# Performance work log

Hardware: AMD Instinct MI355X
Metric: run time of the kernel (lower is better)

## Reference

```python
import jax, jax.numpy as jnp
import numpy as np

B, S, H = 32, 2048, 1024

def setup_inputs() -> dict:
    key = jax.random.key(0)
    k1, k2, k3, k4, k5 = jax.random.split(key, 5)
    return {
        "hidden": jax.random.normal(k1, (B, H), dtype=jnp.float32),
        "encoder_outputs": jax.random.normal(k2, (B, S, H), dtype=jnp.float32),
        "W_attn": jax.random.normal(k3, (H, H), dtype=jnp.float32) * (1.0 / np.sqrt(H)),
        "b_attn": jax.random.normal(k4, (H,), dtype=jnp.float32) * 0.01,
        "v": jax.random.uniform(k5, (H,), dtype=jnp.float32),
    }

def reference(hidden, encoder_outputs, W_attn, b_attn, v):
    # energy = tanh((enc + hidden[:,None,:]) @ W^T + b)  -> [B,S,H]
    x = encoder_outputs + hidden[:, None, :]
    energy = jnp.tanh(jnp.einsum('bsh,oh->bso', x, W_attn) + b_attn)
    scores = jnp.einsum('bsh,h->bs', energy, v)            # [B,S]
    attn_weights = jax.nn.softmax(scores, axis=1)          # [B,S]
    context = jnp.einsum('bs,bsh->bh', attn_weights, encoder_outputs)  # [B,H]
    return (context, attn_weights)
```

## Files before the change

### kernel.cpp

```cpp
#include <hip/hip_runtime.h>
#include <hip/hip_bf16.h>

#define BATCH 32
#define SEQ   2048
#define HID   1024
#define M_TOT (BATCH*SEQ)
#define NG    32

typedef __attribute__((ext_vector_type(8))) short          bf16x8;
typedef __attribute__((ext_vector_type(8))) unsigned short us8;
typedef __attribute__((ext_vector_type(4))) float          f32x4;

__device__ __forceinline__ unsigned short f2bf_rn(float x) {
    unsigned u = __float_as_uint(x);
    return (unsigned short)((u + 0x7fffu + ((u >> 16) & 1u)) >> 16);
}
__device__ __forceinline__ float bf2f(unsigned short h) {
    return __uint_as_float(((unsigned)h) << 16);
}

using as1_cv = const __attribute__((address_space(1))) void;
using as3_v  = __attribute__((address_space(3))) void;
__device__ __forceinline__ void gload16(const void* g, char* s) {
    __builtin_amdgcn_global_load_lds((as1_cv*)g, (as3_v*)s, 16, 0, 0);
}

#define FENCE() asm volatile("" ::: "memory")
#define BAR_LG() do { asm volatile("s_waitcnt lgkmcnt(0)" ::: "memory"); \
                      __builtin_amdgcn_s_barrier(); FENCE(); } while (0)
#define BAR_VM4() do { asm volatile("s_waitcnt vmcnt(4) lgkmcnt(0)" ::: "memory"); \
                       __builtin_amdgcn_s_barrier(); FENCE(); } while (0)

#define MFMA_BLK(A4, B4, IB) do { \
  _Pragma("unroll") for (int i_ = 0; i_ < 4; i_++) \
  _Pragma("unroll") for (int j_ = 0; j_ < 4; j_++) \
    acc[(IB) + i_][j_] = __builtin_amdgcn_mfma_f32_16x16x32_bf16(A4[i_], B4[j_], acc[(IB)+i_][j_], 0, 0, 0); \
} while (0)

__global__ __launch_bounds__(256) void k_convW(const float* __restrict__ W,
                                               unsigned short* __restrict__ w2) {
    const int i8 = (blockIdx.x * 256 + threadIdx.x) * 8;
    const int o = i8 >> 10, h = i8 & 1023;
    float4 w0 = *(const float4*)(W + i8);
    float4 w1 = *(const float4*)(W + i8 + 4);
    float xs[8] = {w0.x, w0.y, w0.z, w0.w, w1.x, w1.y, w1.z, w1.w};
    us8 hv{}, lv{};
#pragma unroll
    for (int t = 0; t < 8; t++) {
        unsigned short xh = f2bf_rn(xs[t]);
        hv[t] = (unsigned short)xh;
        lv[t] = (unsigned short)f2bf_rn(xs[t] - bf2f(xh));
    }
    *(us8*)(w2 + (size_t)o * 2048 + h)        = hv;
    *(us8*)(w2 + (size_t)o * 2048 + 1024 + h) = lv;
}

__global__ __launch_bounds__(512, 2) void k_gemm_scores(
    const float* __restrict__ enc,
    const float* __restrict__ hidden,
    const unsigned short* __restrict__ w2,
    const float* __restrict__ b_attn,
    const float* __restrict__ v,
    float* __restrict__ pscore16)
{
    extern __shared__ char smem[];
    float* hidL = (float*)(smem + 131072);

    const int tid  = threadIdx.x;
    const int lane = tid & 63, wid = tid >> 6;
    const int wr = wid >> 2, wc = wid & 3;
    const int fr = lane & 15, g = lane >> 4;
    const int gxr = (fr >> 1) & 3;
    const int gsw = (g ^ gxr) * 16;

    const int bid  = blockIdx.x;
    const int swz  = (bid & 7) * 128 + (bid >> 3);
    const int mbase = (swz >> 2) * 256;
    const int nbase = (swz & 3) * 256;
    const int bidx  = mbase >> 11;

    const int arow = tid >> 1;
    const int acol = (tid & 1) * 16;
    const int axr  = (arow >> 1) & 3;
    const int ao0  = (((tid & 1) * 2) ^ axr) * 16;
    const int ao1  = ao0 ^ 16;
    const float* encP = enc + (size_t)(mbase + arow) * HID + acol;

    const int brow  = wid * 16 + (lane >> 2);
    const int bsx8  = ((lane & 3) ^ ((lane >> 3) & 3)) * 8;

    *(float2*)(hidL + tid * 2) = *(const float2*)(hidden + (size_t)bidx * HID + tid * 2);

    f32x4 acc[8][4];
#pragma unroll
    for (int i = 0; i < 8; i++)
#pragma unroll
        for (int j = 0; j < 4; j++) acc[i][j] = (f32x4)0.f;

    float4 er[4];

    auto loadEnc = [&](int Gn) {
        const float* ep = encP + Gn * 32;
#pragma unroll
        for (int q = 0; q < 4; q++) er[q] = *(const float4*)(ep + q * 4);
    };
    auto convA = [&](int Gn) {
        char* ap = smem + (Gn & 1) * 32768 + arow * 64;
        const float* hp = hidL + Gn * 32 + acol;
        us8 hv0{}, hv1{}, lv0{}, lv1{};
#pragma unroll
        for (int q = 0; q < 4; q++) {
            float4 e = er[q];
            float4 h = *(const float4*)(hp + q * 4);
            float xs[4] = {e.x + h.x, e.y + h.y, e.z + h.z, e.w + h.w};
#pragma unroll
            for (int t = 0; t < 4; t++) {
                unsigned short xh = f2bf_rn(xs[t]);
                unsigned short xl = f2bf_rn(xs[t] - bf2f(xh));
                const int p = q * 4 + t;
                if (p < 8) { hv0[p] = xh; lv0[p] = xl; }
                else       { hv1[p - 8] = xh; lv1[p - 8] = xl; }
            }
        }
        *(us8*)(ap + ao0)          = hv0;
        *(us8*)(ap + ao1)          = hv1;
        *(us8*)(ap + 16384 + ao0)  = lv0;
        *(us8*)(ap + 16384 + ao1)  = lv1;
    };
    auto stageB = [&](int G2, int part) {
        const unsigned short* s0 = w2 + (size_t)(nbase + brow) * 2048 + part * 1024 + G2 * 32 + bsx8;
        char* d0 = smem + 65536 + (G2 & 1) * 32768 + part * 16384 + wid * 1024;
        gload16(s0, d0);
        gload16(s0 + (size_t)128 * 2048, d0 + 8192);
    };
    auto rdA = [&](int slot, int part, int i) -> bf16x8 {
        return *(const bf16x8*)(smem + slot * 32768 + part * 16384 +
                                (wr * 128 + i * 16 + fr) * 64 + gsw);
    };
    auto rdB = [&](int slot, int part, int j) -> bf16x8 {
        return *(const bf16x8*)(smem + 65536 + slot * 32768 + part * 16384 +
                                (wc * 64 + j * 16 + fr) * 64 + gsw);
    };

    loadEnc(0);
    stageB(0, 0); stageB(0, 1);
    stageB(1, 0); stageB(1, 1);
    asm volatile("s_waitcnt lgkmcnt(0)" ::: "memory");
    __builtin_amdgcn_s_barrier(); FENCE();
    convA(0);
    loadEnc(1);

    bf16x8 aa[4], bh[4], bl[4];

    for (int G = 0; G < NG; ++G) {
        const int slot = G & 1;
        BAR_VM4();
#pragma unroll
        for (int i = 0; i < 4; i++) aa[i] = rdA(slot, 0, i);
#pragma unroll
        for (int j = 0; j < 4; j++) bh[j] = rdB(slot, 0, j);
#pragma unroll
        for (int j = 0; j < 4; j++) bl[j] = rdB(slot, 1, j);
        __builtin_amdgcn_s_setprio(1);
        MFMA_BLK(aa, bh, 0);
        __builtin_amdgcn_s_setprio(0);
        BAR_LG();
        if (G + 2 < NG) stageB(G + 2, 0);
        __builtin_amdgcn_s_setprio(1);
        MFMA_BLK(aa, bl, 0);
        __builtin_amdgcn_s_setprio(0);
        BAR_LG();
#pragma unroll
        for (int i = 0; i < 4; i++) aa[i] = rdA(slot, 0, 4 + i);
        if (G + 2 < NG) stageB(G + 2, 1);
        __builtin_amdgcn_s_setprio(1);
        MFMA_BLK(aa, bh, 4);
        __builtin_amdgcn_s_setprio(0);
        BAR_LG();
        if (G + 1 < NG) convA(G + 1);
        if (G + 2 < NG) loadEnc(G + 2);
        __builtin_amdgcn_s_setprio(1);
        MFMA_BLK(aa, bl, 4);
        __builtin_amdgcn_s_setprio(0);
        BAR_LG();
#pragma unroll
        for (int i = 0; i < 4; i++) aa[i] = rdA(slot, 1, i);
        __builtin_amdgcn_s_setprio(1);
        MFMA_BLK(aa, bh, 0);
        __builtin_amdgcn_s_setprio(0);
        BAR_LG();
#pragma unroll
        for (int i = 0; i < 4; i++) aa[i] = rdA(slot, 1, 4 + i);
        __builtin_amdgcn_s_setprio(1);
        MFMA_BLK(aa, bh, 4);
        __builtin_amdgcn_s_setprio(0);
    }

    float rs[8][4];
#pragma unroll
    for (int i = 0; i < 8; i++)
#pragma unroll
        for (int r = 0; r < 4; r++) rs[i][r] = 0.f;

#pragma unroll
    for (int j = 0; j < 4; j++) {
        const int n = nbase + wc * 64 + j * 16 + fr;
        const float ba = b_attn[n];
        const float vv = v[n];
#pragma unroll
        for (int i = 0; i < 8; i++)
#pragma unroll
            for (int r = 0; r < 4; r++) {
                float e  = acc[i][j][r] + ba;
                float ex = __expf(2.f * e);
                rs[i][r] += (1.f - 2.f / (ex + 1.f)) * vv;
            }
    }
#pragma unroll
    for (int off = 1; off < 16; off <<= 1)
#pragma unroll
        for (int i = 0; i < 8; i++)
#pragma unroll
            for (int r = 0; r < 4; r++) rs[i][r] += __shfl_xor(rs[i][r], off, 64);

    float v0 = 0.f, v1 = 0.f;
#pragma unroll
    for (int i = 0; i < 4; i++)
#pragma unroll
        for (int r = 0; r < 4; r++)
            if (fr == i * 4 + r) { v0 = rs[i][r]; v1 = rs[i + 4][r]; }

    const int plane = (swz & 3) * 4 + wc;
    const size_t pb = (size_t)plane * M_TOT + mbase + wr * 128 + g * 4 + (fr & 3);
    pscore16[pb + (fr >> 2) * 16]      = v0;
    pscore16[pb + (fr >> 2) * 16 + 64] = v1;
}

__global__ __launch_bounds__(256) void k_softmax(const float* __restrict__ ps,
                                                 float* __restrict__ out) {
    const int b = blockIdx.x, t = threadIdx.x;
    __shared__ float red[8];
    float loc[8];
    float lmax = -1e30f;
#pragma unroll
    for (int i = 0; i < 8; i++) {
        const int s = t + i * 256;
        float sc = 0.f;
#pragma unroll
        for (int p = 0; p < 16; p++) sc += ps[(size_t)p * M_TOT + (size_t)b * SEQ + s];
        loc[i] = sc;
        lmax = fmaxf(lmax, sc);
    }
    for (int o = 32; o; o >>= 1) lmax = fmaxf(lmax, __shfl_xor(lmax, o, 64));
    if ((t & 63) == 0) red[t >> 6] = lmax;
    __syncthreads();
    const float bmax = fmaxf(fmaxf(red[0], red[1]), fmaxf(red[2], red[3]));
    float ev[8], lsum = 0.f;
#pragma unroll
    for (int i = 0; i < 8; i++) { ev[i] = expf(loc[i] - bmax); lsum += ev[i]; }
    for (int o = 32; o; o >>= 1) lsum += __shfl_xor(lsum, o, 64);
    __syncthreads();
    if ((t & 63) == 0) red[4 + (t >> 6)] = lsum;
    __syncthreads();
    const float inv = 1.f / (red[4] + red[5] + red[6] + red[7]);
#pragma unroll
    for (int i = 0; i < 8; i++)
        out[(size_t)BATCH * HID + (size_t)b * SEQ + t + i * 256] = ev[i] * inv;
}

__global__ __launch_bounds__(256) void k_pctx(const float* __restrict__ enc,
                                              const float* __restrict__ attn,
                                              float* __restrict__ pctx) {
    const int hc = blockIdx.x, scb = blockIdx.y, b = blockIdx.z;
    const int h = hc * 256 + threadIdx.x;
    const float* ap = attn + (size_t)b * SEQ + scb * 256;
    const float* ep = enc + ((size_t)b * SEQ + scb * 256) * HID + h;
    float a = 0.f;
#pragma unroll 4
    for (int s = 0; s < 256; s++) a += ap[s] * ep[(size_t)s * HID];
    pctx[((size_t)scb * BATCH + b) * HID + h] = a;
}

__global__ __launch_bounds__(256) void k_ctx(const float* __restrict__ pctx,
                                             float* __restrict__ out) {
    const int i = blockIdx.x * 256 + threadIdx.x;
    float a = 0.f;
#pragma unroll
    for (int p = 0; p < 8; p++) a += pctx[(size_t)p * BATCH * HID + i];
    out[i] = a;
}

extern "C" void kernel_launch(void* const* d_in, const int* in_sizes, int n_in,
                              void* d_out, int out_size, void* d_ws, size_t ws_size,
                              hipStream_t stream) {
    const float* hidden = (const float*)d_in[0];
    const float* enc    = (const float*)d_in[1];
    const float* W      = (const float*)d_in[2];
    const float* b_attn = (const float*)d_in[3];
    const float* v      = (const float*)d_in[4];
    float* out = (float*)d_out;

    char* ws = (char*)d_ws;
    unsigned short* w2 = (unsigned short*)ws;
    float* pscore16    = (float*)(ws + ((size_t)4 << 20));
    float* pctx        = (float*)ws;

    const int smemBytes = 131072 + 4096;
    hipFuncSetAttribute((const void*)k_gemm_scores,
                        hipFuncAttributeMaxDynamicSharedMemorySize, smemBytes);

    k_convW<<<dim3(512), dim3(256), 0, stream>>>(W, w2);
    k_gemm_scores<<<dim3(1024), dim3(512), smemBytes, stream>>>(
        enc, hidden, w2, b_attn, v, pscore16);
    k_softmax<<<dim3(BATCH), dim3(256), 0, stream>>>(pscore16, out);
    k_pctx<<<dim3(4, 8, BATCH), dim3(256), 0, stream>>>(enc, out + BATCH * HID, pctx);
    k_ctx<<<dim3(128), dim3(256), 0, stream>>>(pctx, out);
}
```

Baseline: 453.5 us.

## Loosen barriers, double-buffer A fragments, and use packed bf16 conversion

The bf16 hi/lo split of the A tile now uses the hardware packed v_cvt_pk_bf16_f32 instruction in place of scalar bit-manipulation rounding. Inside the main loop, several barriers no longer wait on lgkmcnt(0) and one barrier is removed entirely. A second A-fragment register set lets LDS reads overlap with the MFMAs that are still running. Loads and stages are now issued every iteration (clamped indices, so redundant ones occur at the tail) so the vmcnt(8) wait count stays uniform. The changes aim to cut conversion ALU work and barrier stalls, at the cost of more registers, redundant tail loads, and a race risk if the weaker barriers fail to order the LDS writes from convA before the later reads.

```diff
diff --git a/kernel.cpp b/kernel.cpp
--- a/kernel.cpp
+++ b/kernel.cpp
@@ -18,6 +18,11 @@
 __device__ __forceinline__ float bf2f(unsigned short h) {
     return __uint_as_float(((unsigned)h) << 16);
 }
+__device__ __forceinline__ unsigned cvt_pk_bf16(float s0, float s1) {
+    unsigned r;
+    asm("v_cvt_pk_bf16_f32 %0, %1, %2" : "=v"(r) : "v"(s0), "v"(s1));
+    return r;
+}
 
 using as1_cv = const __attribute__((address_space(1))) void;
 using as3_v  = __attribute__((address_space(3))) void;
@@ -26,9 +31,10 @@
 }
 
 #define FENCE() asm volatile("" ::: "memory")
+#define BAR_P()  do { FENCE(); __builtin_amdgcn_s_barrier(); FENCE(); } while (0)
 #define BAR_LG() do { asm volatile("s_waitcnt lgkmcnt(0)" ::: "memory"); \
                       __builtin_amdgcn_s_barrier(); FENCE(); } while (0)
-#define BAR_VM4() do { asm volatile("s_waitcnt vmcnt(4) lgkmcnt(0)" ::: "memory"); \
+#define BAR_VM8() do { asm volatile("s_waitcnt vmcnt(8) lgkmcnt(0)" ::: "memory"); \
                        __builtin_amdgcn_s_barrier(); FENCE(); } while (0)
 
 #define MFMA_BLK(A4, B4, IB) do { \
@@ -107,25 +113,28 @@
     auto convA = [&](int Gn) {
         char* ap = smem + (Gn & 1) * 32768 + arow * 64;
         const float* hp = hidL + Gn * 32 + acol;
-        us8 hv0{}, hv1{}, lv0{}, lv1{};
+        unsigned hpk[8], lpk[8];
 #pragma unroll
         for (int q = 0; q < 4; q++) {
             float4 e = er[q];
             float4 h = *(const float4*)(hp + q * 4);
-            float xs[4] = {e.x + h.x, e.y + h.y, e.z + h.z, e.w + h.w};
-#pragma unroll
-            for (int t = 0; t < 4; t++) {
-                unsigned short xh = f2bf_rn(xs[t]);
-                unsigned short xl = f2bf_rn(xs[t] - bf2f(xh));
-                const int p = q * 4 + t;
-                if (p < 8) { hv0[p] = xh; lv0[p] = xl; }
-                else       { hv1[p - 8] = xh; lv1[p - 8] = xl; }
-            }
+            float x0 = e.x + h.x, x1 = e.y + h.y;
+            float x2 = e.z + h.z, x3 = e.w + h.w;
+            unsigned p01 = cvt_pk_bf16(x0, x1);
+            unsigned p23 = cvt_pk_bf16(x2, x3);
+            float h0 = __uint_as_float(p01 << 16);
+            float h1 = __uint_as_float(p01 & 0xffff0000u);
+            float h2 = __uint_as_float(p23 << 16);
+            float h3 = __uint_as_float(p23 & 0xffff0000u);
+            hpk[q * 2]     = p01;
+            hpk[q * 2 + 1] = p23;
+            lpk[q * 2]     = cvt_pk_bf16(x0 - h0, x1 - h1);
+            lpk[q * 2 + 1] = cvt_pk_bf16(x2 - h2, x3 - h3);
         }
-        *(us8*)(ap + ao0)          = hv0;
-        *(us8*)(ap + ao1)          = hv1;
-        *(us8*)(ap + 16384 + ao0)  = lv0;
-        *(us8*)(ap + 16384 + ao1)  = lv1;
+        *(uint4*)(ap + ao0)          = make_uint4(hpk[0], hpk[1], hpk[2], hpk[3]);
+        *(uint4*)(ap + ao1)          = make_uint4(hpk[4], hpk[5], hpk[6], hpk[7]);
+        *(uint4*)(ap + 16384 + ao0)  = make_uint4(lpk[0], lpk[1], lpk[2], lpk[3]);
+        *(uint4*)(ap + 16384 + ao1)  = make_uint4(lpk[4], lpk[5], lpk[6], lpk[7]);
     };
     auto stageB = [&](int G2, int part) {
         const unsigned short* s0 = w2 + (size_t)(nbase + brow) * 2048 + part * 1024 + G2 * 32 + bsx8;
@@ -150,11 +159,13 @@
     convA(0);
     loadEnc(1);
 
-    bf16x8 aa[4], bh[4], bl[4];
+    bf16x8 aa[4], aa2[4], bh[4], bl[4];
 
     for (int G = 0; G < NG; ++G) {
         const int slot = G & 1;
-        BAR_VM4();
+        const int Gs = (G + 2 < NG) ? G + 2 : G;
+        const int Ge = (G + 2 < NG) ? G + 2 : NG - 1;
+        BAR_VM8();
 #pragma unroll
         for (int i = 0; i < 4; i++) aa[i] = rdA(slot, 0, i);
 #pragma unroll
@@ -165,34 +176,33 @@
         MFMA_BLK(aa, bh, 0);
         __builtin_amdgcn_s_setprio(0);
         BAR_LG();
-        if (G + 2 < NG) stageB(G + 2, 0);
+        stageB(Gs, 0);
         __builtin_amdgcn_s_setprio(1);
         MFMA_BLK(aa, bl, 0);
         __builtin_amdgcn_s_setprio(0);
-        BAR_LG();
-#pragma unroll
-        for (int i = 0; i < 4; i++) aa[i] = rdA(slot, 0, 4 + i);
-        if (G + 2 < NG) stageB(G + 2, 1);
-        __builtin_amdgcn_s_setprio(1);
-        MFMA_BLK(aa, bh, 4);
-        __builtin_amdgcn_s_setprio(0);
-        BAR_LG();
+        BAR_P();
+#pragma unroll
+        for (int i = 0; i < 4; i++) aa2[i] = rdA(slot, 0, 4 + i);
+        stageB(Gs, 1);
+        __builtin_amdgcn_s_setprio(1);
+        MFMA_BLK(aa2, bh, 4);
+        __builtin_amdgcn_s_setprio(0);
+        BAR_P();
         if (G + 1 < NG) convA(G + 1);
-        if (G + 2 < NG) loadEnc(G + 2);
-        __builtin_amdgcn_s_setprio(1);
-        MFMA_BLK(aa, bl, 4);
-        __builtin_amdgcn_s_setprio(0);
-        BAR_LG();
+        loadEnc(Ge);
+        __builtin_amdgcn_s_setprio(1);
+        MFMA_BLK(aa2, bl, 4);
+        __builtin_amdgcn_s_setprio(0);
+        BAR_P();
 #pragma unroll
         for (int i = 0; i < 4; i++) aa[i] = rdA(slot, 1, i);
         __builtin_amdgcn_s_setprio(1);
         MFMA_BLK(aa, bh, 0);
         __builtin_amdgcn_s_setprio(0);
-        BAR_LG();
-#pragma unroll
-        for (int i = 0; i < 4; i++) aa[i] = rdA(slot, 1, 4 + i);
-        __builtin_amdgcn_s_setprio(1);
-        MFMA_BLK(aa, bh, 4);
+#pragma unroll
+        for (int i = 0; i < 4; i++) aa2[i] = rdA(slot, 1, 4 + i);
+        __builtin_amdgcn_s_setprio(1);
+        MFMA_BLK(aa2, bh, 4);
         __builtin_amdgcn_s_setprio(0);
     }
 
```

New measurement: 405.1 us. 1.12x faster.
